# Performance work log

Hardware: AMD Instinct MI355X
Metric: run time of the kernel (lower is better)

Reference implementation:

```python
import jax, jax.numpy as jnp
import numpy as np

B, S, H, NH = 2, 2048, 1024, 16
DK = H // NH


def setup_inputs() -> dict:
    key = jax.random.key(0)
    ks = jax.random.split(key, 11)
    sc = 1.0 / np.sqrt(H)
    return {
        "q": jax.random.normal(ks[0], (B, S, H), jnp.float32),
        "v": jax.random.normal(ks[1], (B, S, H), jnp.float32),
        "k": jax.random.normal(ks[2], (B, S, H), jnp.float32),
        "Wq": jax.random.normal(ks[3], (H, H), jnp.float32) * sc,
        "bq": jax.random.normal(ks[4], (H,), jnp.float32) * 0.01,
        "Wk": jax.random.normal(ks[5], (H, H), jnp.float32) * sc,
        "bk": jax.random.normal(ks[6], (H,), jnp.float32) * 0.01,
        "Wv": jax.random.normal(ks[7], (H, H), jnp.float32) * sc,
        "bv": jax.random.normal(ks[8], (H,), jnp.float32) * 0.01,
        "Wo": jax.random.normal(ks[9], (H, H), jnp.float32) * sc,
        "bo": jax.random.normal(ks[10], (H,), jnp.float32) * 0.01,
    }


def reference(q, v, k, Wq, bq, Wk, bk, Wv, bv, Wo, bo):
    b, s, h = q.shape
    # projections; torch Linear computes x @ W.T + b
    qh = (q @ Wq.T + bq).reshape(b, s, NH, DK).transpose(0, 2, 1, 3)  # [B,NH,S,DK]
    kh = (k @ Wk.T + bk).reshape(b, s, NH, DK).transpose(0, 2, 1, 3)
    vh = (v @ Wv.T + bv).reshape(b, s, NH, DK).transpose(0, 2, 1, 3)
    scores = jnp.einsum("bhqd,bhkd->bhqk", qh, kh) / jnp.sqrt(
        jnp.asarray(DK, qh.dtype))  # [B,NH,S,S]
    probs = jax.nn.softmax(scores, axis=-1)
    ctx = jnp.einsum("bhqk,bhkd->bhqd", probs, vh)  # [B,NH,S,DK]
    concat = ctx.transpose(0, 2, 1, 3).reshape(b, s, h)
    return concat @ Wo.T + bo
```

## Files before the change

kernel.cpp:

```cpp
#include <hip/hip_runtime.h>
#include <cstddef>
#include <cstdint>

typedef _Float16 f16x8 __attribute__((ext_vector_type(8)));
typedef _Float16 f16x4 __attribute__((ext_vector_type(4)));
typedef __fp16   h16x2 __attribute__((ext_vector_type(2)));
typedef float    f32x4 __attribute__((ext_vector_type(4)));
typedef float    f32x2 __attribute__((ext_vector_type(2)));

constexpr int B_  = 2;
constexpr int S_  = 2048;
constexpr int H_  = 1024;
constexpr int NH_ = 16;
constexpr int DK_ = 64;
constexpr int M_  = B_ * S_;
constexpr int K_  = H_;

constexpr float SOFF = 4.0f;

#define MFMA32(a, b, c) __builtin_amdgcn_mfma_f32_16x16x32_f16((a), (b), (c), 0, 0, 0)

__device__ __forceinline__ void glds16(const void* g, void* l) {
    __builtin_amdgcn_global_load_lds(
        (const __attribute__((address_space(1))) void*)g,
        (__attribute__((address_space(3))) void*)l, 16, 0, 0);
}

struct CvtArgs {
    const float* s[7];
    _Float16*    d[7];
    int          n[7];
};

__global__ __launch_bounds__(256) void cvt7(CvtArgs a)
{
    const int seg = blockIdx.y;
    const int i = (blockIdx.x * 256 + threadIdx.x) * 8;
    if (i + 8 <= a.n[seg]) {
        const float4 v0 = *reinterpret_cast<const float4*>(a.s[seg] + i);
        const float4 v1 = *reinterpret_cast<const float4*>(a.s[seg] + i + 4);
        f16x8 o;
        o[0] = (_Float16)v0.x; o[1] = (_Float16)v0.y;
        o[2] = (_Float16)v0.z; o[3] = (_Float16)v0.w;
        o[4] = (_Float16)v1.x; o[5] = (_Float16)v1.y;
        o[6] = (_Float16)v1.z; o[7] = (_Float16)v1.w;
        *reinterpret_cast<f16x8*>(a.d[seg] + i) = o;
    }
}

struct QkvArgs {
    const _Float16* A[3];
    const _Float16* W[3];
    const float*    bias[3];
    _Float16* dstQ;
    _Float16* dstK;
    _Float16* dstV;
    float qscale;
};

__global__ __launch_bounds__(256) void gemm_qkv(QkvArgs args)
{
    constexpr int BM = 128, BN = 128, BK = 32;
    __shared__ __align__(16) _Float16 sm[8192];
    auto As = reinterpret_cast<_Float16(*)[BK]>(sm);
    auto Ws = reinterpret_cast<_Float16(*)[BK]>(sm + 4096);
    auto Tr = reinterpret_cast<_Float16(*)[64]>(sm);

    const int z = blockIdx.z;
    const _Float16* __restrict__ A = args.A[z];
    const _Float16* __restrict__ W = args.W[z];
    const float* __restrict__ bias = args.bias[z];

    const int t = threadIdx.x;
    const int w = t >> 6, lane = t & 63, quad = lane >> 4, l16 = lane & 15;
    const int m0 = blockIdx.y * BM;
    const int n0 = blockIdx.x * BN;
    const int wr = (w & 1) * 64, wc = (w >> 1) * 64;
    const int srow = lane >> 2, scol = (lane & 3) * 8;

    f32x4 acc[4][4];
#pragma unroll
    for (int i = 0; i < 4; ++i)
#pragma unroll
        for (int j = 0; j < 4; ++j) acc[i][j] = (f32x4){0.f, 0.f, 0.f, 0.f};

    for (int k0 = 0; k0 < K_; k0 += BK) {
        glds16(&A[(size_t)(m0 + w * 32 + srow) * K_ + k0 + scol], &As[w * 32][0]);
        glds16(&A[(size_t)(m0 + w * 32 + 16 + srow) * K_ + k0 + scol], &As[w * 32 + 16][0]);
        glds16(&W[(size_t)(n0 + w * 32 + srow) * K_ + k0 + scol], &Ws[w * 32][0]);
        glds16(&W[(size_t)(n0 + w * 32 + 16 + srow) * K_ + k0 + scol], &Ws[w * 32 + 16][0]);
        __syncthreads();

        f16x8 af[4], bf[4];
#pragma unroll
        for (int i = 0; i < 4; ++i)
            af[i] = *reinterpret_cast<const f16x8*>(&As[wr + i * 16 + l16][quad * 8]);
#pragma unroll
        for (int j = 0; j < 4; ++j)
            bf[j] = *reinterpret_cast<const f16x8*>(&Ws[wc + j * 16 + l16][quad * 8]);
#pragma unroll
        for (int i = 0; i < 4; ++i)
#pragma unroll
            for (int j = 0; j < 4; ++j)
                acc[i][j] = MFMA32(af[i], bf[j], acc[i][j]);
        __syncthreads();
    }

    const float scale = (z == 0) ? args.qscale : 1.0f;
    float bv[4];
#pragma unroll
    for (int j = 0; j < 4; ++j) bv[j] = bias[n0 + wc + j * 16 + l16];

    if (z == 2) {
#pragma unroll
        for (int i = 0; i < 4; ++i) {
            const int sb = m0 + wr + i * 16 + quad * 4;
            const int b = sb >> 11, s = sb & (S_ - 1);
            const int kt = s >> 4;
            const int w4 = kt & 3, tIdx = kt >> 2;
            const int p16 = tIdx >> 1, sub = tIdx & 1;
#pragma unroll
            for (int j = 0; j < 4; ++j) {
                const int d = wc + j * 16 + l16;
                const int h = blockIdx.x * 2 + (d >> 6);
                const int dt = (d & 63) >> 4;
                f16x4 ov;
#pragma unroll
                for (int r = 0; r < 4; ++r) ov[r] = (_Float16)(acc[i][j][r] + bv[j]);
                _Float16* base = args.dstV + ((size_t)b * NH_ + h) * 131072
                    + (size_t)(((w4 * 16 + p16) * 4 + dt) * 512 + lane * 8 + sub * 4);
                *reinterpret_cast<f16x4*>(base) = ov;
            }
        }
        return;
    }

    _Float16* dst = (z == 0) ? args.dstQ : args.dstK;
    const int b = m0 >> 11, s0 = m0 & (S_ - 1);
#pragma unroll
    for (int ch = 0; ch < 2; ++ch) {
        __syncthreads();
        if ((w >> 1) == ch) {
#pragma unroll
            for (int i = 0; i < 4; ++i)
#pragma unroll
                for (int j = 0; j < 4; ++j)
#pragma unroll
                    for (int r = 0; r < 4; ++r)
                        Tr[wr + i * 16 + quad * 4 + r][j * 16 + l16] =
                            (_Float16)((acc[i][j][r] + bv[j]) * scale);
        }
        __syncthreads();
        const int h = blockIdx.x * 2 + ch;
        _Float16* dbase = dst + ((size_t)(b * NH_ + h) * S_ + s0) * DK_;
#pragma unroll
        for (int p = 0; p < 4; ++p) {
            const int c = t + p * 256;
            *reinterpret_cast<f16x8*>(&dbase[c * 8]) =
                *reinterpret_cast<const f16x8*>(&Tr[c >> 3][(c & 7) * 8]);
        }
    }
}

__global__ __launch_bounds__(256) void gemm_out(
    const _Float16* __restrict__ A, const _Float16* __restrict__ W,
    const float* __restrict__ bias, float* __restrict__ out)
{
    constexpr int BM = 64, BN = 128, BK = 32;
    __shared__ _Float16 As[BM][BK];
    __shared__ _Float16 Ws[BN][BK];

    const int t = threadIdx.x;
    const int w = t >> 6, lane = t & 63, quad = lane >> 4, l16 = lane & 15;
    const int m0 = blockIdx.y * BM;
    const int n0 = blockIdx.x * BN;
    const int wc = w * 32;
    const int srow = lane >> 2, scol = (lane & 3) * 8;

    f32x4 acc[4][2];
#pragma unroll
    for (int i = 0; i < 4; ++i)
#pragma unroll
        for (int j = 0; j < 2; ++j) acc[i][j] = (f32x4){0.f, 0.f, 0.f, 0.f};

    for (int k0 = 0; k0 < K_; k0 += BK) {
        glds16(&A[(size_t)(m0 + w * 16 + srow) * K_ + k0 + scol], &As[w * 16][0]);
        glds16(&W[(size_t)(n0 + w * 32 + srow) * K_ + k0 + scol], &Ws[w * 32][0]);
        glds16(&W[(size_t)(n0 + w * 32 + 16 + srow) * K_ + k0 + scol], &Ws[w * 32 + 16][0]);
        __syncthreads();

        f16x8 af[4], bf[2];
#pragma unroll
        for (int i = 0; i < 4; ++i)
            af[i] = *reinterpret_cast<const f16x8*>(&As[i * 16 + l16][quad * 8]);
#pragma unroll
        for (int j = 0; j < 2; ++j)
            bf[j] = *reinterpret_cast<const f16x8*>(&Ws[wc + j * 16 + l16][quad * 8]);
#pragma unroll
        for (int i = 0; i < 4; ++i)
#pragma unroll
            for (int j = 0; j < 2; ++j)
                acc[i][j] = MFMA32(af[i], bf[j], acc[i][j]);
        __syncthreads();
    }

    float bvv[2];
#pragma unroll
    for (int j = 0; j < 2; ++j) bvv[j] = bias[n0 + wc + j * 16 + l16];

#pragma unroll
    for (int i = 0; i < 4; ++i)
#pragma unroll
        for (int j = 0; j < 2; ++j)
#pragma unroll
            for (int r = 0; r < 4; ++r)
                out[(size_t)(m0 + i * 16 + quad * 4 + r) * H_ +
                    n0 + wc + j * 16 + l16] = acc[i][j][r] + bvv[j];
}

__global__ __launch_bounds__(256) void attn_mfma(
    const _Float16* __restrict__ qh, const _Float16* __restrict__ kh,
    const _Float16* __restrict__ vfrag, _Float16* __restrict__ ctx)
{
    __shared__ float Ob[4][64][36];
    __shared__ float Ls[4][64];
    __shared__ float Linv[64];

    const int t = threadIdx.x;
    const int w = t >> 6, lane = t & 63, quad = lane >> 4, l16 = lane & 15;

    const int lin = blockIdx.x;
    const int xcd = lin & 7, slot = lin >> 3;
    const int bh = xcd + 8 * (slot >> 5);
    const int q0 = (slot & 31) * 64;

    const _Float16* qb = qh + (size_t)bh * S_ * DK_;
    const _Float16* kb = kh + (size_t)bh * S_ * DK_;
    const _Float16* vb = vfrag + (size_t)bh * 131072;

    f16x8 qf[4][2];
#pragma unroll
    for (int qt = 0; qt < 4; ++qt)
#pragma unroll
        for (int h2 = 0; h2 < 2; ++h2)
            qf[qt][h2] = *reinterpret_cast<const f16x8*>(
                &qb[(size_t)(q0 + qt * 16 + l16) * DK_ + h2 * 32 + quad * 8]);

    const f32x4 msoff = (f32x4){-SOFF, -SOFF, -SOFF, -SOFF};

    f32x4 o[4][4];
#pragma unroll
    for (int dt = 0; dt < 4; ++dt)
#pragma unroll
        for (int qt = 0; qt < 4; ++qt) o[dt][qt] = (f32x4){0.f, 0.f, 0.f, 0.f};
    f32x2 lp2[4];
#pragma unroll
    for (int qt = 0; qt < 4; ++qt) lp2[qt] = (f32x2){0.f, 0.f};

    const _Float16* kp = kb + (size_t)(w * 16 + l16) * DK_ + quad * 8;
    const _Float16* vp = vb + (size_t)w * 32768 + lane * 8;

    f32x4 scA[4], scB[4];
    {
        const f16x8 kA0 = *reinterpret_cast<const f16x8*>(kp);
        const f16x8 kA1 = *reinterpret_cast<const f16x8*>(kp + 32);
        const f16x8 kB0 = *reinterpret_cast<const f16x8*>(kp + 64 * DK_);
        const f16x8 kB1 = *reinterpret_cast<const f16x8*>(kp + 64 * DK_ + 32);
        kp += 128 * DK_;
#pragma unroll
        for (int qt = 0; qt < 4; ++qt) {
            f32x4 t0 = MFMA32(kA0, qf[qt][0], msoff);
            scA[qt] = MFMA32(kA1, qf[qt][1], t0);
            f32x4 t1 = MFMA32(kB0, qf[qt][0], msoff);
            scB[qt] = MFMA32(kB1, qf[qt][1], t1);
        }
    }

    for (int p = 0; p < 16; ++p) {
        const _Float16* nk = (p < 15) ? kp : (kp - 128 * DK_);
        const f16x8 nA0 = *reinterpret_cast<const f16x8*>(nk);
        const f16x8 nA1 = *reinterpret_cast<const f16x8*>(nk + 32);
        const f16x8 nB0 = *reinterpret_cast<const f16x8*>(nk + 64 * DK_);
        const f16x8 nB1 = *reinterpret_cast<const f16x8*>(nk + 64 * DK_ + 32);
        kp = nk + 128 * DK_;

        f16x8 vf8[4];
#pragma unroll
        for (int dt = 0; dt < 4; ++dt)
            vf8[dt] = *reinterpret_cast<const f16x8*>(vp + dt * 512);
        vp += 2048;

        f16x8 pf8[4];
#pragma unroll
        for (int qt = 0; qt < 4; ++qt) {
            const float a0 = __builtin_amdgcn_exp2f(scA[qt][0]);
            const float a1 = __builtin_amdgcn_exp2f(scA[qt][1]);
            const float a2 = __builtin_amdgcn_exp2f(scA[qt][2]);
            const float a3 = __builtin_amdgcn_exp2f(scA[qt][3]);
            const float b0 = __builtin_amdgcn_exp2f(scB[qt][0]);
            const float b1 = __builtin_amdgcn_exp2f(scB[qt][1]);
            const float b2 = __builtin_amdgcn_exp2f(scB[qt][2]);
            const float b3 = __builtin_amdgcn_exp2f(scB[qt][3]);
            lp2[qt] += ((f32x2){a0, a1} + (f32x2){a2, a3}) +
                       ((f32x2){b0, b1} + (f32x2){b2, b3});
            h16x2* ph = reinterpret_cast<h16x2*>(&pf8[qt]);
            ph[0] = __builtin_amdgcn_cvt_pkrtz(a0, a1);
            ph[1] = __builtin_amdgcn_cvt_pkrtz(a2, a3);
            ph[2] = __builtin_amdgcn_cvt_pkrtz(b0, b1);
            ph[3] = __builtin_amdgcn_cvt_pkrtz(b2, b3);
        }

        __builtin_amdgcn_s_setprio(1);
#pragma unroll
        for (int dt = 0; dt < 4; ++dt)
#pragma unroll
            for (int qt = 0; qt < 4; ++qt)
                o[dt][qt] = MFMA32(vf8[dt], pf8[qt], o[dt][qt]);
#pragma unroll
        for (int qt = 0; qt < 4; ++qt) {
            f32x4 t0 = MFMA32(nA0, qf[qt][0], msoff);
            scA[qt] = MFMA32(nA1, qf[qt][1], t0);
            f32x4 t1 = MFMA32(nB0, qf[qt][0], msoff);
            scB[qt] = MFMA32(nB1, qf[qt][1], t1);
        }
        __builtin_amdgcn_s_setprio(0);
    }

#pragma unroll
    for (int qt = 0; qt < 4; ++qt) {
        float l = lp2[qt][0] + lp2[qt][1];
        l += __shfl_xor(l, 16);
        l += __shfl_xor(l, 32);
        if (quad == 0) Ls[w][qt * 16 + l16] = l;
    }
    __syncthreads();
    if (t < 64)
        Linv[t] = 1.f / (((Ls[0][t] + Ls[1][t]) + (Ls[2][t] + Ls[3][t])));

    const int b = bh >> 4, hh = bh & 15;
    const int dg = t & 3, qq = t >> 2;
#pragma unroll
    for (int ph = 0; ph < 2; ++ph) {
        __syncthreads();
#pragma unroll
        for (int dl = 0; dl < 2; ++dl) {
            const int dt = ph * 2 + dl;
#pragma unroll
            for (int qt = 0; qt < 4; ++qt)
                *reinterpret_cast<f32x4*>(
                    &Ob[w][qt * 16 + l16][dl * 16 + quad * 4]) = o[dt][qt];
        }
        __syncthreads();
        f32x4 s0 = (f32x4){0.f, 0.f, 0.f, 0.f};
        f32x4 s1 = (f32x4){0.f, 0.f, 0.f, 0.f};
#pragma unroll
        for (int ww = 0; ww < 4; ++ww) {
            s0 += *reinterpret_cast<const f32x4*>(&Ob[ww][qq][dg * 8]);
            s1 += *reinterpret_cast<const f32x4*>(&Ob[ww][qq][dg * 8 + 4]);
        }
        const float li = Linv[qq];
        f16x8 ov;
#pragma unroll
        for (int r = 0; r < 4; ++r) {
            ov[r]     = (_Float16)(s0[r] * li);
            ov[4 + r] = (_Float16)(s1[r] * li);
        }
        *reinterpret_cast<f16x8*>(
            &ctx[((size_t)b * S_ + q0 + qq) * H_ + hh * 64 + ph * 32 + dg * 8]) = ov;
    }
}

extern "C" void kernel_launch(void* const* d_in, const int* in_sizes, int n_in,
                              void* d_out, int out_size, void* d_ws,
                              size_t ws_size, hipStream_t stream)
{
    (void)in_sizes; (void)n_in; (void)out_size; (void)ws_size;
    const float* q  = (const float*)d_in[0];
    const float* v  = (const float*)d_in[1];
    const float* k  = (const float*)d_in[2];
    const float* Wq = (const float*)d_in[3];
    const float* bq = (const float*)d_in[4];
    const float* Wk = (const float*)d_in[5];
    const float* bk = (const float*)d_in[6];
    const float* Wv = (const float*)d_in[7];
    const float* bv = (const float*)d_in[8];
    const float* Wo = (const float*)d_in[9];
    const float* bo = (const float*)d_in[10];
    float* out = (float*)d_out;

    constexpr size_t NACT = (size_t)M_ * K_;
    constexpr size_t NW   = (size_t)H_ * H_;
    _Float16* p = (_Float16*)d_ws;
    _Float16* q16  = p;
    _Float16* k16  = p + NACT;
    _Float16* v16  = p + 2 * NACT;
    _Float16* w16q = p + 3 * NACT;
    _Float16* w16k = w16q + NW;
    _Float16* w16v = w16k + NW;
    _Float16* w16o = w16v + NW;
    _Float16* qhd  = w16o + NW;
    _Float16* khd  = qhd + NACT;
    _Float16* vfr  = khd + NACT;
    _Float16* ctx  = q16;

    CvtArgs ca;
    ca.s[0] = q;  ca.d[0] = q16;  ca.n[0] = (int)NACT;
    ca.s[1] = v;  ca.d[1] = v16;  ca.n[1] = (int)NACT;
    ca.s[2] = k;  ca.d[2] = k16;  ca.n[2] = (int)NACT;
    ca.s[3] = Wq; ca.d[3] = w16q; ca.n[3] = (int)NW;
    ca.s[4] = Wk; ca.d[4] = w16k; ca.n[4] = (int)NW;
    ca.s[5] = Wv; ca.d[5] = w16v; ca.n[5] = (int)NW;
    ca.s[6] = Wo; ca.d[6] = w16o; ca.n[6] = (int)NW;
    cvt7<<<dim3(2048, 7), 256, 0, stream>>>(ca);

    QkvArgs ga;
    ga.A[0] = q16;  ga.W[0] = w16q; ga.bias[0] = bq;
    ga.A[1] = k16;  ga.W[1] = w16k; ga.bias[1] = bk;
    ga.A[2] = v16;  ga.W[2] = w16v; ga.bias[2] = bv;
    ga.dstQ = qhd;  ga.dstK = khd;  ga.dstV = vfr;
    ga.qscale = 0.125f * 1.4426950408889634f;

    gemm_qkv<<<dim3(H_ / 128, M_ / 128, 3), 256, 0, stream>>>(ga);

    attn_mfma<<<dim3(S_ / 64 * B_ * NH_), 256, 0, stream>>>(qhd, khd, vfr, ctx);

    gemm_out<<<dim3(H_ / 128, M_ / 64), 256, 0, stream>>>(ctx, w16o, bo, out);
}
```

Before: 225.9 us.

## Compact cvt grid, split V fragment layout into halves, reorder MFMA groups

The conversion kernel now runs on a flat grid of 8192 blocks and maps block ids to segments by hand. This removes the 7x2048 grid in which most weight-segment blocks did nothing but fail the bounds check. The V fragment layout written by the QKV GEMM is changed so each lane stores and loads two 4-element halves 256 elements apart instead of one contiguous 8-element run, which changes the global access pattern in attention. In the attention loop, the next-tile QK score MFMAs are issued before the PV MFMAs, which may change how dependencies and latency are hidden.

```diff
diff --git a/kernel.cpp b/kernel.cpp
--- a/kernel.cpp
+++ b/kernel.cpp
@@ -29,23 +29,23 @@
 struct CvtArgs {
     const float* s[7];
     _Float16*    d[7];
-    int          n[7];
 };
 
 __global__ __launch_bounds__(256) void cvt7(CvtArgs a)
 {
-    const int seg = blockIdx.y;
-    const int i = (blockIdx.x * 256 + threadIdx.x) * 8;
-    if (i + 8 <= a.n[seg]) {
-        const float4 v0 = *reinterpret_cast<const float4*>(a.s[seg] + i);
-        const float4 v1 = *reinterpret_cast<const float4*>(a.s[seg] + i + 4);
-        f16x8 o;
-        o[0] = (_Float16)v0.x; o[1] = (_Float16)v0.y;
-        o[2] = (_Float16)v0.z; o[3] = (_Float16)v0.w;
-        o[4] = (_Float16)v1.x; o[5] = (_Float16)v1.y;
-        o[6] = (_Float16)v1.z; o[7] = (_Float16)v1.w;
-        *reinterpret_cast<f16x8*>(a.d[seg] + i) = o;
-    }
+    const int bid = blockIdx.x;
+    int seg, blk;
+    if (bid < 6144) { seg = bid >> 11;               blk = bid & 2047; }
+    else            { seg = 3 + ((bid - 6144) >> 9); blk = (bid - 6144) & 511; }
+    const int i = (blk * 256 + threadIdx.x) * 8;
+    const float4 v0 = *reinterpret_cast<const float4*>(a.s[seg] + i);
+    const float4 v1 = *reinterpret_cast<const float4*>(a.s[seg] + i + 4);
+    f16x8 o;
+    o[0] = (_Float16)v0.x; o[1] = (_Float16)v0.y;
+    o[2] = (_Float16)v0.z; o[3] = (_Float16)v0.w;
+    o[4] = (_Float16)v1.x; o[5] = (_Float16)v1.y;
+    o[6] = (_Float16)v1.z; o[7] = (_Float16)v1.w;
+    *reinterpret_cast<f16x8*>(a.d[seg] + i) = o;
 }
 
 struct QkvArgs {
@@ -128,7 +128,7 @@
 #pragma unroll
                 for (int r = 0; r < 4; ++r) ov[r] = (_Float16)(acc[i][j][r] + bv[j]);
                 _Float16* base = args.dstV + ((size_t)b * NH_ + h) * 131072
-                    + (size_t)(((w4 * 16 + p16) * 4 + dt) * 512 + lane * 8 + sub * 4);
+                    + (size_t)(((w4 * 16 + p16) * 4 + dt) * 512 + sub * 256 + lane * 4);
                 *reinterpret_cast<f16x4*>(base) = ov;
             }
         }
@@ -258,7 +258,7 @@
     for (int qt = 0; qt < 4; ++qt) lp2[qt] = (f32x2){0.f, 0.f};
 
     const _Float16* kp = kb + (size_t)(w * 16 + l16) * DK_ + quad * 8;
-    const _Float16* vp = vb + (size_t)w * 32768 + lane * 8;
+    const _Float16* vp = vb + (size_t)w * 32768 + lane * 4;
 
     f32x4 scA[4], scB[4];
     {
@@ -286,8 +286,12 @@
 
         f16x8 vf8[4];
 #pragma unroll
-        for (int dt = 0; dt < 4; ++dt)
-            vf8[dt] = *reinterpret_cast<const f16x8*>(vp + dt * 512);
+        for (int dt = 0; dt < 4; ++dt) {
+            const f16x4 lo = *reinterpret_cast<const f16x4*>(vp + dt * 512);
+            const f16x4 hi = *reinterpret_cast<const f16x4*>(vp + dt * 512 + 256);
+            reinterpret_cast<f16x4*>(&vf8[dt])[0] = lo;
+            reinterpret_cast<f16x4*>(&vf8[dt])[1] = hi;
+        }
         vp += 2048;
 
         f16x8 pf8[4];
@@ -312,17 +316,17 @@
 
         __builtin_amdgcn_s_setprio(1);
 #pragma unroll
-        for (int dt = 0; dt < 4; ++dt)
-#pragma unroll
-            for (int qt = 0; qt < 4; ++qt)
-                o[dt][qt] = MFMA32(vf8[dt], pf8[qt], o[dt][qt]);
-#pragma unroll
         for (int qt = 0; qt < 4; ++qt) {
             f32x4 t0 = MFMA32(nA0, qf[qt][0], msoff);
             scA[qt] = MFMA32(nA1, qf[qt][1], t0);
             f32x4 t1 = MFMA32(nB0, qf[qt][0], msoff);
             scB[qt] = MFMA32(nB1, qf[qt][1], t1);
         }
+#pragma unroll
+        for (int dt = 0; dt < 4; ++dt)
+#pragma unroll
+            for (int qt = 0; qt < 4; ++qt)
+                o[dt][qt] = MFMA32(vf8[dt], pf8[qt], o[dt][qt]);
         __builtin_amdgcn_s_setprio(0);
     }
 
@@ -404,14 +408,14 @@
     _Float16* ctx  = q16;
 
     CvtArgs ca;
-    ca.s[0] = q;  ca.d[0] = q16;  ca.n[0] = (int)NACT;
-    ca.s[1] = v;  ca.d[1] = v16;  ca.n[1] = (int)NACT;
-    ca.s[2] = k;  ca.d[2] = k16;  ca.n[2] = (int)NACT;
-    ca.s[3] = Wq; ca.d[3] = w16q; ca.n[3] = (int)NW;
-    ca.s[4] = Wk; ca.d[4] = w16k; ca.n[4] = (int)NW;
-    ca.s[5] = Wv; ca.d[5] = w16v; ca.n[5] = (int)NW;
-    ca.s[6] = Wo; ca.d[6] = w16o; ca.n[6] = (int)NW;
-    cvt7<<<dim3(2048, 7), 256, 0, stream>>>(ca);
+    ca.s[0] = q;  ca.d[0] = q16;
+    ca.s[1] = v;  ca.d[1] = v16;
+    ca.s[2] = k;  ca.d[2] = k16;
+    ca.s[3] = Wq; ca.d[3] = w16q;
+    ca.s[4] = Wk; ca.d[4] = w16k;
+    ca.s[5] = Wv; ca.d[5] = w16v;
+    ca.s[6] = Wo; ca.d[6] = w16o;
+    cvt7<<<dim3(8192), 256, 0, stream>>>(ca);
 
     QkvArgs ga;
     ga.A[0] = q16;  ga.W[0] = w16q; ga.bias[0] = bq;
```

After: 228.9 us. No clear change (+1.3%).

## Fuse fp32-to-fp16 activation conversion into QKV GEMM tile loads

Applied to the files above, without the earlier changes.

Removes the separate conversion pass over the q/k/v activations. The QKV GEMM now streams fp32 activations straight into an XOR-swizzled LDS tile and converts them to fp16 in registers before the MFMA. The conversion kernel only handles the four weight matrices, which cuts a full read and write of about 24 MB of activations. In exchange, global loads and LDS traffic for A double and each k-step does more conversion instructions, and LDS use grows from 16 KB to 24 KB per block.

```diff
diff --git a/kernel.cpp b/kernel.cpp
--- a/kernel.cpp
+++ b/kernel.cpp
@@ -27,29 +27,26 @@
 }
 
 struct CvtArgs {
-    const float* s[7];
-    _Float16*    d[7];
-    int          n[7];
+    const float* s[4];
+    _Float16*    d[4];
 };
 
 __global__ __launch_bounds__(256) void cvt7(CvtArgs a)
 {
-    const int seg = blockIdx.y;
-    const int i = (blockIdx.x * 256 + threadIdx.x) * 8;
-    if (i + 8 <= a.n[seg]) {
-        const float4 v0 = *reinterpret_cast<const float4*>(a.s[seg] + i);
-        const float4 v1 = *reinterpret_cast<const float4*>(a.s[seg] + i + 4);
-        f16x8 o;
-        o[0] = (_Float16)v0.x; o[1] = (_Float16)v0.y;
-        o[2] = (_Float16)v0.z; o[3] = (_Float16)v0.w;
-        o[4] = (_Float16)v1.x; o[5] = (_Float16)v1.y;
-        o[6] = (_Float16)v1.z; o[7] = (_Float16)v1.w;
-        *reinterpret_cast<f16x8*>(a.d[seg] + i) = o;
-    }
+    const int seg = blockIdx.x >> 9, blk = blockIdx.x & 511;
+    const int i = (blk * 256 + threadIdx.x) * 8;
+    const float4 v0 = *reinterpret_cast<const float4*>(a.s[seg] + i);
+    const float4 v1 = *reinterpret_cast<const float4*>(a.s[seg] + i + 4);
+    f16x8 o;
+    o[0] = (_Float16)v0.x; o[1] = (_Float16)v0.y;
+    o[2] = (_Float16)v0.z; o[3] = (_Float16)v0.w;
+    o[4] = (_Float16)v1.x; o[5] = (_Float16)v1.y;
+    o[6] = (_Float16)v1.z; o[7] = (_Float16)v1.w;
+    *reinterpret_cast<f16x8*>(a.d[seg] + i) = o;
 }
 
 struct QkvArgs {
-    const _Float16* A[3];
+    const float*    A[3];
     const _Float16* W[3];
     const float*    bias[3];
     _Float16* dstQ;
@@ -61,13 +58,13 @@
 __global__ __launch_bounds__(256) void gemm_qkv(QkvArgs args)
 {
     constexpr int BM = 128, BN = 128, BK = 32;
-    __shared__ __align__(16) _Float16 sm[8192];
-    auto As = reinterpret_cast<_Float16(*)[BK]>(sm);
-    auto Ws = reinterpret_cast<_Float16(*)[BK]>(sm + 4096);
-    auto Tr = reinterpret_cast<_Float16(*)[64]>(sm);
+    __shared__ __align__(16) char smraw[24576];
+    float*    As = reinterpret_cast<float*>(smraw);
+    _Float16* Ws = reinterpret_cast<_Float16*>(smraw + 16384);
+    auto Tr = reinterpret_cast<_Float16(*)[64]>(smraw);
 
     const int z = blockIdx.z;
-    const _Float16* __restrict__ A = args.A[z];
+    const float* __restrict__ A = args.A[z];
     const _Float16* __restrict__ W = args.W[z];
     const float* __restrict__ bias = args.bias[z];
 
@@ -76,7 +73,11 @@
     const int m0 = blockIdx.y * BM;
     const int n0 = blockIdx.x * BN;
     const int wr = (w & 1) * 64, wc = (w >> 1) * 64;
-    const int srow = lane >> 2, scol = (lane & 3) * 8;
+
+    const int srowA = lane >> 3;
+    const int scolA = ((lane & 7) ^ srowA) * 4;
+    const int srowW = lane >> 2, scolW = (lane & 3) * 8;
+    const int px = l16 & 7;
 
     f32x4 acc[4][4];
 #pragma unroll
@@ -85,19 +86,36 @@
         for (int j = 0; j < 4; ++j) acc[i][j] = (f32x4){0.f, 0.f, 0.f, 0.f};
 
     for (int k0 = 0; k0 < K_; k0 += BK) {
-        glds16(&A[(size_t)(m0 + w * 32 + srow) * K_ + k0 + scol], &As[w * 32][0]);
-        glds16(&A[(size_t)(m0 + w * 32 + 16 + srow) * K_ + k0 + scol], &As[w * 32 + 16][0]);
-        glds16(&W[(size_t)(n0 + w * 32 + srow) * K_ + k0 + scol], &Ws[w * 32][0]);
-        glds16(&W[(size_t)(n0 + w * 32 + 16 + srow) * K_ + k0 + scol], &Ws[w * 32 + 16][0]);
+#pragma unroll
+        for (int c = 0; c < 4; ++c) {
+            const int r0 = w * 32 + c * 8;
+            glds16(&A[(size_t)(m0 + r0 + srowA) * K_ + k0 + scolA],
+                   As + r0 * 32);
+        }
+        glds16(&W[(size_t)(n0 + w * 32 + srowW) * K_ + k0 + scolW],
+               Ws + (w * 32) * 32);
+        glds16(&W[(size_t)(n0 + w * 32 + 16 + srowW) * K_ + k0 + scolW],
+               Ws + (w * 32 + 16) * 32);
         __syncthreads();
 
         f16x8 af[4], bf[4];
 #pragma unroll
-        for (int i = 0; i < 4; ++i)
-            af[i] = *reinterpret_cast<const f16x8*>(&As[wr + i * 16 + l16][quad * 8]);
+        for (int i = 0; i < 4; ++i) {
+            const char* ab = reinterpret_cast<const char*>(As) +
+                             (wr + i * 16 + l16) * 128;
+            const f32x4 a0 = *reinterpret_cast<const f32x4*>(
+                ab + ((quad * 2) ^ px) * 16);
+            const f32x4 a1 = *reinterpret_cast<const f32x4*>(
+                ab + ((quad * 2 + 1) ^ px) * 16);
+            af[i][0] = (_Float16)a0[0]; af[i][1] = (_Float16)a0[1];
+            af[i][2] = (_Float16)a0[2]; af[i][3] = (_Float16)a0[3];
+            af[i][4] = (_Float16)a1[0]; af[i][5] = (_Float16)a1[1];
+            af[i][6] = (_Float16)a1[2]; af[i][7] = (_Float16)a1[3];
+        }
 #pragma unroll
         for (int j = 0; j < 4; ++j)
-            bf[j] = *reinterpret_cast<const f16x8*>(&Ws[wc + j * 16 + l16][quad * 8]);
+            bf[j] = *reinterpret_cast<const f16x8*>(
+                &Ws[(wc + j * 16 + l16) * 32 + quad * 8]);
 #pragma unroll
         for (int i = 0; i < 4; ++i)
 #pragma unroll
@@ -391,32 +409,26 @@
     constexpr size_t NACT = (size_t)M_ * K_;
     constexpr size_t NW   = (size_t)H_ * H_;
     _Float16* p = (_Float16*)d_ws;
-    _Float16* q16  = p;
-    _Float16* k16  = p + NACT;
-    _Float16* v16  = p + 2 * NACT;
-    _Float16* w16q = p + 3 * NACT;
+    _Float16* w16q = p;
     _Float16* w16k = w16q + NW;
     _Float16* w16v = w16k + NW;
     _Float16* w16o = w16v + NW;
     _Float16* qhd  = w16o + NW;
     _Float16* khd  = qhd + NACT;
     _Float16* vfr  = khd + NACT;
-    _Float16* ctx  = q16;
+    _Float16* ctx  = vfr + NACT;
 
     CvtArgs ca;
-    ca.s[0] = q;  ca.d[0] = q16;  ca.n[0] = (int)NACT;
-    ca.s[1] = v;  ca.d[1] = v16;  ca.n[1] = (int)NACT;
-    ca.s[2] = k;  ca.d[2] = k16;  ca.n[2] = (int)NACT;
-    ca.s[3] = Wq; ca.d[3] = w16q; ca.n[3] = (int)NW;
-    ca.s[4] = Wk; ca.d[4] = w16k; ca.n[4] = (int)NW;
-    ca.s[5] = Wv; ca.d[5] = w16v; ca.n[5] = (int)NW;
-    ca.s[6] = Wo; ca.d[6] = w16o; ca.n[6] = (int)NW;
-    cvt7<<<dim3(2048, 7), 256, 0, stream>>>(ca);
+    ca.s[0] = Wq; ca.d[0] = w16q;
+    ca.s[1] = Wk; ca.d[1] = w16k;
+    ca.s[2] = Wv; ca.d[2] = w16v;
+    ca.s[3] = Wo; ca.d[3] = w16o;
+    cvt7<<<dim3(2048), 256, 0, stream>>>(ca);
 
     QkvArgs ga;
-    ga.A[0] = q16;  ga.W[0] = w16q; ga.bias[0] = bq;
-    ga.A[1] = k16;  ga.W[1] = w16k; ga.bias[1] = bk;
-    ga.A[2] = v16;  ga.W[2] = w16v; ga.bias[2] = bv;
+    ga.A[0] = q;    ga.W[0] = w16q; ga.bias[0] = bq;
+    ga.A[1] = k;    ga.W[1] = w16k; ga.bias[1] = bk;
+    ga.A[2] = v;    ga.W[2] = w16v; ga.bias[2] = bv;
     ga.dstQ = qhd;  ga.dstK = khd;  ga.dstV = vfr;
     ga.qscale = 0.125f * 1.4426950408889634f;
 
```

New measurement: 234.0 us. 3.6% more time.
